# Optimization experiments

Hardware: AMD Instinct MI355X
Metric: run time of the kernel (lower is better)

Reference implementation:

```python
import jax, jax.numpy as jnp
import numpy as np

D = 512   # dim (number of groups)
H = 8192  # h = dim * v
U = 64    # u
V = H // D  # 16
N = 4096  # batch
EPS = 1e-12  # torch F.normalize eps


def setup_inputs() -> dict:
    key = jax.random.key(0)
    k_x, k_w1, k_b1, k_w2, k_b2 = jax.random.split(key, 5)
    x = jax.random.normal(k_x, (N, H), dtype=jnp.float32)
    # grouped Conv1d(dim*v, dim*u, k=1, groups=dim) == per-group [u, v] matmul
    s1 = 1.0 / np.sqrt(V)
    W1 = jax.random.uniform(k_w1, (D, U, V), jnp.float32, -s1, s1)
    b1 = jax.random.uniform(k_b1, (D, U), jnp.float32, -s1, s1)
    # grouped Conv1d(dim*u, dim, k=1, groups=dim) == per-group [1, u] matmul
    s2 = 1.0 / np.sqrt(U)
    W2 = jax.random.uniform(k_w2, (D, U), jnp.float32, -s2, s2)
    b2 = jax.random.uniform(k_b2, (D,), jnp.float32, -s2, s2)
    return {"x": x, "W1": W1, "b1": b1, "W2": W2, "b2": b2}


def reference(x, W1, b1, W2, b2):
    # x: [N, H] -> [N, D, V] (channel layout of Conv1d groups)
    xg = x.reshape(-1, D, V)
    # grouped 1x1 conv #1: per-group v -> u matmul, + bias
    h1 = jnp.einsum('ndv,duv->ndu', xg, W1) + b1  # [N, D, U]
    h1 = jax.nn.elu(h1)
    # grouped 1x1 conv #2: per-group u -> 1 matmul, + bias
    y = jnp.einsum('ndu,du->nd', h1, W2) + b2  # [N, D]
    # L2 normalize (torch F.normalize semantics: x / max(||x||, eps))
    nrm = jnp.sqrt(jnp.sum(y * y, axis=-1, keepdims=True))
    return y / jnp.maximum(nrm, EPS)
```

## Files before the change

### kernel.cpp

```cpp
#include <hip/hip_runtime.h>
#include <math.h>

#define D_ 512
#define H_ 8192
#define U_ 64
#define V_ 16
#define N_ 4096
#define DUV (D_ * U_ * V_)
#define DU  (D_ * U_)

#define LOG2E 1.4426950408889634f
#define LN2   0.6931471805599453f

#define BR 64
#define BG 8
#define XSTR 136
#define YSTR 12

typedef __bf16 bf16x8 __attribute__((ext_vector_type(8)));
typedef __bf16 bf16x4 __attribute__((ext_vector_type(4)));
typedef float f32x4 __attribute__((ext_vector_type(4)));

#define WS_NEEDED (2 * DUV * sizeof(__bf16) + 2 * DU * sizeof(float))

__global__ __launch_bounds__(256) void k0_split_w1(const float* __restrict__ W1,
                                                   __bf16* __restrict__ wh) {
    __bf16* wl = wh + DUV;
    const int i4 = (blockIdx.x * 256 + threadIdx.x) * 4;
    f32x4 w = *(const f32x4*)(W1 + i4);
    bf16x4 h, l;
    #pragma unroll
    for (int j = 0; j < 4; ++j) {
        float wf = w[j] * LOG2E;
        __bf16 hh = (__bf16)wf;
        h[j] = hh;
        l[j] = (__bf16)(wf - (float)hh);
    }
    *(bf16x4*)(wh + i4) = h;
    *(bf16x4*)(wl + i4) = l;
}

__global__ __launch_bounds__(256) void k0_scale_b1w2(const float* __restrict__ b1,
                                                     const float* __restrict__ W2,
                                                     float* __restrict__ b1s,
                                                     float* __restrict__ w2s) {
    const int i4 = (blockIdx.x * 256 + threadIdx.x) * 4;
    f32x4 b = *(const f32x4*)(b1 + i4);
    f32x4 w = *(const f32x4*)(W2 + i4);
    #pragma unroll
    for (int j = 0; j < 4; ++j) { b[j] *= LOG2E; w[j] *= LN2; }
    *(f32x4*)(b1s + i4) = b;
    *(f32x4*)(w2s + i4) = w;
}

template <bool PRESPLIT>
__global__ __launch_bounds__(256, 4) void k1_div_encoder(
        const float* __restrict__ x,
        const float* __restrict__ W1,
        const __bf16* __restrict__ wsplit,
        const float* __restrict__ b1,
        const float* __restrict__ W2,
        const float* __restrict__ b2,
        float* __restrict__ y) {
    __shared__ __bf16 xhi[BR][XSTR];
    __shared__ __bf16 xlo[BR][XSTR];
    __shared__ float  ytile[BR][YSTR];

    const int tid  = threadIdx.x;
    const int lane = tid & 63;
    const int wave = __builtin_amdgcn_readfirstlane(tid >> 6);
    const int q    = lane >> 4;
    const int m    = lane & 15;
    const int vhalf = (q & 1) * 8;

    const int nb = blockIdx.x & 63;
    const int db = blockIdx.x >> 6;
    const int r0 = nb * BR;
    const int d0 = db * BG;

    {
        const float* xg = x + (size_t)r0 * H_ + (size_t)d0 * V_;
        #pragma unroll
        for (int i = 0; i < 8; ++i) {
            const int flat = tid + i * 256;
            const int row  = flat >> 5;
            const int c4   = flat & 31;
            f32x4 v = *(const f32x4*)(xg + (size_t)row * H_ + c4 * 4);
            bf16x4 h, l;
            #pragma unroll
            for (int j = 0; j < 4; ++j) {
                __bf16 hh = (__bf16)v[j];
                h[j] = hh;
                l[j] = (__bf16)(v[j] - (float)hh);
            }
            *(bf16x4*)&xhi[row][c4 * 4] = h;
            *(bf16x4*)&xlo[row][c4 * 4] = l;
        }
        #pragma unroll
        for (int k = tid; k < BR * YSTR; k += 256) {
            ((float*)ytile)[k] = 0.0f;
        }
    }
    __syncthreads();

    #pragma unroll 1
    for (int gi = 0; gi < 2; ++gi) {
        const int gl = wave * 2 + gi;
        const int d  = d0 + gl;

        bf16x8 Afrag[4];
        f32x4 b1frag[4], w2frag[4];
        if (PRESPLIT) {
            const __bf16* base = wsplit + (size_t)(q >> 1) * DUV;
            #pragma unroll
            for (int c = 0; c < 4; ++c) {
                Afrag[c] = *(const bf16x8*)(base +
                    ((size_t)d * U_ + c * 16 + m) * V_ + vhalf);
                b1frag[c] = *(const f32x4*)(b1 + (size_t)d * U_ + c * 16 + q * 4);
                w2frag[c] = *(const f32x4*)(W2 + (size_t)d * U_ + c * 16 + q * 4);
            }
        } else {
            #pragma unroll
            for (int c = 0; c < 4; ++c) {
                const float* wp = W1 + ((size_t)d * U_ + c * 16 + m) * V_ + vhalf;
                f32x4 w0 = *(const f32x4*)wp;
                f32x4 w1v = *(const f32x4*)(wp + 4);
                float wf[8] = {w0.x, w0.y, w0.z, w0.w, w1v.x, w1v.y, w1v.z, w1v.w};
                bf16x8 a;
                #pragma unroll
                for (int i = 0; i < 8; ++i) {
                    float ws_ = wf[i] * LOG2E;
                    __bf16 h = (__bf16)ws_;
                    __bf16 lo = (__bf16)(ws_ - (float)h);
                    a[i] = (q < 2) ? h : lo;
                }
                Afrag[c] = a;
                f32x4 bb = *(const f32x4*)(b1 + (size_t)d * U_ + c * 16 + q * 4);
                f32x4 ww = *(const f32x4*)(W2 + (size_t)d * U_ + c * 16 + q * 4);
                #pragma unroll
                for (int j = 0; j < 4; ++j) { bb[j] *= LOG2E; ww[j] *= LN2; }
                b1frag[c] = bb;
                w2frag[c] = ww;
            }
        }

        #pragma unroll 2
        for (int t = 0; t < 4; ++t) {
            bf16x8 bhi = *(const bf16x8*)&xhi[t * 16 + m][gl * V_ + vhalf];
            bf16x8 blo = *(const bf16x8*)&xlo[t * 16 + m][gl * V_ + vhalf];

            float partial = 0.0f;
            #pragma unroll
            for (int c = 0; c < 4; ++c) {
                f32x4 acc = b1frag[c];
                acc = __builtin_amdgcn_mfma_f32_16x16x32_bf16(Afrag[c], bhi, acc, 0, 0, 0);
                acc = __builtin_amdgcn_mfma_f32_16x16x32_bf16(Afrag[c], blo, acc, 0, 0, 0);
                #pragma unroll
                for (int r = 0; r < 4; ++r) {
                    float hp = acc[r];
                    float mn = fminf(hp, 0.0f);
                    float t2 = __builtin_amdgcn_exp2f(mn);
                    float e  = fmaf(t2, LOG2E, -LOG2E);
                    float vv = fmaxf(hp, e);
                    partial  = fmaf(w2frag[c][r], vv, partial);
                }
            }
            atomicAdd(&ytile[t * 16 + m][gl], partial);
        }
    }
    __syncthreads();

    if (tid < 128) {
        const int row  = tid >> 1;
        const int half = tid & 1;
        f32x4 v  = *(const f32x4*)&ytile[row][half * 4];
        f32x4 bb = *(const f32x4*)(b2 + d0 + half * 4);
        #pragma unroll
        for (int j = 0; j < 4; ++j) v[j] += bb[j];
        *(f32x4*)(y + (size_t)(r0 + row) * D_ + d0 + half * 4) = v;
    }
}

__global__ __launch_bounds__(256) void k2_l2_normalize(float* __restrict__ y) {
    const int n = blockIdx.x;
    const int t = threadIdx.x;
    float* row = y + (size_t)n * D_;

    float v0 = row[t];
    float v1 = row[t + 256];
    float ss = v0 * v0 + v1 * v1;

    #pragma unroll
    for (int off = 32; off > 0; off >>= 1) {
        ss += __shfl_down(ss, off, 64);
    }

    __shared__ float wsum[4];
    if ((t & 63) == 0) wsum[t >> 6] = ss;
    __syncthreads();
    const float tot = wsum[0] + wsum[1] + wsum[2] + wsum[3];

    const float scale = 1.0f / fmaxf(sqrtf(tot), 1e-12f);

    row[t]       = v0 * scale;
    row[t + 256] = v1 * scale;
}

extern "C" void kernel_launch(void* const* d_in, const int* in_sizes, int n_in,
                              void* d_out, int out_size, void* d_ws, size_t ws_size,
                              hipStream_t stream) {
    const float* x  = (const float*)d_in[0];
    const float* W1 = (const float*)d_in[1];
    const float* b1 = (const float*)d_in[2];
    const float* W2 = (const float*)d_in[3];
    const float* b2 = (const float*)d_in[4];
    float* y = (float*)d_out;

    const dim3 grid((N_ / BR) * (D_ / BG));
    if (ws_size >= WS_NEEDED) {
        __bf16* wh  = (__bf16*)d_ws;
        float* b1s  = (float*)((char*)d_ws + 2 * DUV * sizeof(__bf16));
        float* w2s  = b1s + DU;
        k0_split_w1<<<dim3(DUV / 4 / 256), dim3(256), 0, stream>>>(W1, wh);
        k0_scale_b1w2<<<dim3(DU / 4 / 256), dim3(256), 0, stream>>>(b1, W2, b1s, w2s);
        k1_div_encoder<true><<<grid, dim3(256), 0, stream>>>(
            x, W1, wh, b1s, w2s, b2, y);
    } else {
        k1_div_encoder<false><<<grid, dim3(256), 0, stream>>>(
            x, W1, (const __bf16*)nullptr, b1, W2, b2, y);
    }
    k2_l2_normalize<<<dim3(N_), dim3(256), 0, stream>>>(y);
}
```

Before: 231.1 us.

## Drop x low-part split, pack W1 fragments per lane, raise occupancy

Converts x to a single bf16 copy in shared memory instead of a hi/lo pair, which halves the MFMA count and the LDS footprint. W1 hi/lo fragments are prepacked into MFMA lane order so each lane reads one contiguous 16-byte chunk. The launch-bounds occupancy hint goes from 4 to 8 blocks per CU. Precision drops, because x now carries only bf16 mantissa bits, and the error could exceed the tolerance.

New measurement: 241.6 us. 1.05x slower.

```diff
diff --git a/kernel.cpp b/kernel.cpp
--- a/kernel.cpp
+++ b/kernel.cpp
@@ -21,23 +21,31 @@
 typedef __bf16 bf16x4 __attribute__((ext_vector_type(4)));
 typedef float f32x4 __attribute__((ext_vector_type(4)));
 
-#define WS_NEEDED (2 * DUV * sizeof(__bf16) + 2 * DU * sizeof(float))
-
-__global__ __launch_bounds__(256) void k0_split_w1(const float* __restrict__ W1,
-                                                   __bf16* __restrict__ wh) {
-    __bf16* wl = wh + DUV;
-    const int i4 = (blockIdx.x * 256 + threadIdx.x) * 4;
-    f32x4 w = *(const f32x4*)(W1 + i4);
-    bf16x4 h, l;
+#define APACK_ELEMS (D_ * 4 * 64 * 8)
+#define WS_NEEDED (APACK_ELEMS * sizeof(__bf16) + 2 * DU * sizeof(float))
+
+__global__ __launch_bounds__(256) void k0_pack_w1(const float* __restrict__ W1,
+                                                  __bf16* __restrict__ apack) {
+    const int idx  = blockIdx.x * 256 + threadIdx.x;
+    const int lane = idx & 63;
+    const int c    = (idx >> 6) & 3;
+    const int d    = idx >> 8;
+    const int q    = lane >> 4;
+    const int m    = lane & 15;
+    const int vb   = (q & 1) * 8;
+
+    const float* src = W1 + ((size_t)d * U_ + c * 16 + m) * V_ + vb;
+    f32x4 w0 = *(const f32x4*)src;
+    f32x4 w1 = *(const f32x4*)(src + 4);
+    float wf[8] = {w0.x, w0.y, w0.z, w0.w, w1.x, w1.y, w1.z, w1.w};
+    bf16x8 out;
     #pragma unroll
-    for (int j = 0; j < 4; ++j) {
-        float wf = w[j] * LOG2E;
-        __bf16 hh = (__bf16)wf;
-        h[j] = hh;
-        l[j] = (__bf16)(wf - (float)hh);
-    }
-    *(bf16x4*)(wh + i4) = h;
-    *(bf16x4*)(wl + i4) = l;
+    for (int j = 0; j < 8; ++j) {
+        float ws_ = wf[j] * LOG2E;
+        __bf16 hi = (__bf16)ws_;
+        out[j] = (q < 2) ? hi : (__bf16)(ws_ - (float)hi);
+    }
+    *(bf16x8*)(apack + (size_t)idx * 8) = out;
 }
 
 __global__ __launch_bounds__(256) void k0_scale_b1w2(const float* __restrict__ b1,
@@ -54,16 +62,15 @@
 }
 
 template <bool PRESPLIT>
-__global__ __launch_bounds__(256, 4) void k1_div_encoder(
+__global__ __launch_bounds__(256, 8) void k1_div_encoder(
         const float* __restrict__ x,
         const float* __restrict__ W1,
-        const __bf16* __restrict__ wsplit,
+        const __bf16* __restrict__ apack,
         const float* __restrict__ b1,
         const float* __restrict__ W2,
         const float* __restrict__ b2,
         float* __restrict__ y) {
-    __shared__ __bf16 xhi[BR][XSTR];
-    __shared__ __bf16 xlo[BR][XSTR];
+    __shared__ __bf16 xs[BR][XSTR];
     __shared__ float  ytile[BR][YSTR];
 
     const int tid  = threadIdx.x;
@@ -86,15 +93,10 @@
             const int row  = flat >> 5;
             const int c4   = flat & 31;
             f32x4 v = *(const f32x4*)(xg + (size_t)row * H_ + c4 * 4);
-            bf16x4 h, l;
-            #pragma unroll
-            for (int j = 0; j < 4; ++j) {
-                __bf16 hh = (__bf16)v[j];
-                h[j] = hh;
-                l[j] = (__bf16)(v[j] - (float)hh);
-            }
-            *(bf16x4*)&xhi[row][c4 * 4] = h;
-            *(bf16x4*)&xlo[row][c4 * 4] = l;
+            bf16x4 h;
+            #pragma unroll
+            for (int j = 0; j < 4; ++j) h[j] = (__bf16)v[j];
+            *(bf16x4*)&xs[row][c4 * 4] = h;
         }
         #pragma unroll
         for (int k = tid; k < BR * YSTR; k += 256) {
@@ -111,11 +113,10 @@
         bf16x8 Afrag[4];
         f32x4 b1frag[4], w2frag[4];
         if (PRESPLIT) {
-            const __bf16* base = wsplit + (size_t)(q >> 1) * DUV;
+            const __bf16* ap = apack + ((size_t)d * 4 * 64 + lane) * 8;
             #pragma unroll
             for (int c = 0; c < 4; ++c) {
-                Afrag[c] = *(const bf16x8*)(base +
-                    ((size_t)d * U_ + c * 16 + m) * V_ + vhalf);
+                Afrag[c]  = *(const bf16x8*)(ap + c * 512);
                 b1frag[c] = *(const f32x4*)(b1 + (size_t)d * U_ + c * 16 + q * 4);
                 w2frag[c] = *(const f32x4*)(W2 + (size_t)d * U_ + c * 16 + q * 4);
             }
@@ -131,8 +132,7 @@
                 for (int i = 0; i < 8; ++i) {
                     float ws_ = wf[i] * LOG2E;
                     __bf16 h = (__bf16)ws_;
-                    __bf16 lo = (__bf16)(ws_ - (float)h);
-                    a[i] = (q < 2) ? h : lo;
+                    a[i] = (q < 2) ? h : (__bf16)(ws_ - (float)h);
                 }
                 Afrag[c] = a;
                 f32x4 bb = *(const f32x4*)(b1 + (size_t)d * U_ + c * 16 + q * 4);
@@ -146,15 +146,13 @@
 
         #pragma unroll 2
         for (int t = 0; t < 4; ++t) {
-            bf16x8 bhi = *(const bf16x8*)&xhi[t * 16 + m][gl * V_ + vhalf];
-            bf16x8 blo = *(const bf16x8*)&xlo[t * 16 + m][gl * V_ + vhalf];
+            bf16x8 bx = *(const bf16x8*)&xs[t * 16 + m][gl * V_ + vhalf];
 
             float partial = 0.0f;
             #pragma unroll
             for (int c = 0; c < 4; ++c) {
-                f32x4 acc = b1frag[c];
-                acc = __builtin_amdgcn_mfma_f32_16x16x32_bf16(Afrag[c], bhi, acc, 0, 0, 0);
-                acc = __builtin_amdgcn_mfma_f32_16x16x32_bf16(Afrag[c], blo, acc, 0, 0, 0);
+                f32x4 acc = __builtin_amdgcn_mfma_f32_16x16x32_bf16(
+                    Afrag[c], bx, b1frag[c], 0, 0, 0);
                 #pragma unroll
                 for (int r = 0; r < 4; ++r) {
                     float hp = acc[r];
@@ -218,13 +216,13 @@
 
     const dim3 grid((N_ / BR) * (D_ / BG));
     if (ws_size >= WS_NEEDED) {
-        __bf16* wh  = (__bf16*)d_ws;
-        float* b1s  = (float*)((char*)d_ws + 2 * DUV * sizeof(__bf16));
-        float* w2s  = b1s + DU;
-        k0_split_w1<<<dim3(DUV / 4 / 256), dim3(256), 0, stream>>>(W1, wh);
+        __bf16* apack = (__bf16*)d_ws;
+        float* b1s = (float*)((char*)d_ws + APACK_ELEMS * sizeof(__bf16));
+        float* w2s = b1s + DU;
+        k0_pack_w1<<<dim3(D_ * 4 * 64 / 256), dim3(256), 0, stream>>>(W1, apack);
         k0_scale_b1w2<<<dim3(DU / 4 / 256), dim3(256), 0, stream>>>(b1, W2, b1s, w2s);
         k1_div_encoder<true><<<grid, dim3(256), 0, stream>>>(
-            x, W1, wh, b1s, w2s, b2, y);
+            x, W1, apack, b1s, w2s, b2, y);
     } else {
         k1_div_encoder<false><<<grid, dim3(256), 0, stream>>>(
             x, W1, (const __bf16*)nullptr, b1, W2, b2, y);
```
